# Optimization experiments

Hardware: AMD Instinct MI355X
Metric: run time of the kernel (lower is better)

## Reference

```python
import jax, jax.numpy as jnp
import numpy as np

N_NODES = 100000
N_EDGES = 1600000
D_IN, D_HID, D_OUT = 64, 64, 32


def _glorot(key, shape):
    fan_in, fan_out = shape[0], shape[1]
    lim = np.sqrt(6.0 / (fan_in + fan_out)).astype(np.float32)
    return jax.random.uniform(key, shape, jnp.float32, -lim, lim)


def setup_inputs() -> dict:
    key = jax.random.key(0)
    ks = jax.random.split(key, 12)
    x = jax.random.normal(ks[0], (N_NODES, D_IN), jnp.float32)
    edge_index = jax.random.randint(ks[1], (2, N_EDGES), 0, N_NODES, jnp.int64)
    return {
        "x": x,
        "edge_index": edge_index,
        # SAGEConv 1 (in->hid): lin_l (aggregated neighbors, with bias), lin_r (root, no bias)
        "Wl1": _glorot(ks[2], (D_IN, D_HID)),
        "Wr1": _glorot(ks[3], (D_IN, D_HID)),
        "b1": jnp.zeros((D_HID,), jnp.float32),
        # SAGEConv 2 (hid->out)
        "Wl2": _glorot(ks[4], (D_HID, D_OUT)),
        "Wr2": _glorot(ks[5], (D_HID, D_OUT)),
        "b2": jnp.zeros((D_OUT,), jnp.float32),
        # trust head: Linear(32,16) -> ReLU -> Linear(16,1) -> Sigmoid (dropout inert in eval)
        "Wt1": _glorot(ks[6], (D_OUT, 16)),
        "bt1": jnp.zeros((16,), jnp.float32),
        "Wt2": _glorot(ks[7], (16, 1)),
        "bt2": jnp.zeros((1,), jnp.float32),
    }


def _sage_conv(x, src, dst, Wl, Wr, b):
    # mean-aggregate neighbor messages: msg flows src -> dst
    msg = x[src]                                              # [E, d] gather
    agg_sum = jax.ops.segment_sum(msg, dst, num_segments=N_NODES)
    deg = jax.ops.segment_sum(jnp.ones((src.shape[0],), x.dtype), dst,
                              num_segments=N_NODES)
    agg = agg_sum / jnp.maximum(deg, 1.0)[:, None]            # zero-degree -> 0
    return agg @ Wl + x @ Wr + b


def reference(x, edge_index, Wl1, Wr1, b1, Wl2, Wr2, b2, Wt1, bt1, Wt2, bt2):
    src, dst = edge_index[0], edge_index[1]
    h = _sage_conv(x, src, dst, Wl1, Wr1, b1)
    h = jax.nn.relu(h)                    # dropout p=0.3 inert in eval
    h = _sage_conv(h, src, dst, Wl2, Wr2, b2)
    t = jax.nn.relu(h @ Wt1 + bt1)        # dropout p=0.2 inert in eval
    trust = jax.nn.sigmoid(t @ Wt2 + bt2)
    return h, trust
```

## Files before the change

### kernel.cpp

```cpp
#include <hip/hip_runtime.h>
#include <math.h>


#define NBUCK   1563
#define BCAP    1536
#define BKCHUNK 4096

__device__ inline unsigned short f2bf(float x) {
    unsigned u = __float_as_uint(x);
    unsigned r = u + 0x7fffu + ((u >> 16) & 1u);
    return (unsigned short)(r >> 16);
}
__device__ inline unsigned pack2(float a, float b) {
    return (unsigned)f2bf(a) | ((unsigned)f2bf(b) << 16);
}
__device__ inline float bflo(unsigned u) { return __uint_as_float(u << 16); }
__device__ inline float bfhi(unsigned u) { return __uint_as_float(u & 0xffff0000u); }

__global__ __launch_bounds__(256) void k_m1(
    const float* __restrict__ x,
    const float* __restrict__ Wl1, const float* __restrict__ Wr1,
    const float* __restrict__ b1,
    unsigned* __restrict__ u16b, float* __restrict__ v,
    const int* __restrict__ src, const int* __restrict__ dst,
    int* __restrict__ gcnt, unsigned* __restrict__ pairs,
    int N, int E, int GB, int BKB)
{
    __shared__ __align__(16) char smem[33792];
    int tid = threadIdx.x;
    int g = blockIdx.x / 5, r5 = blockIdx.x % 5;

    if (r5 == 4) {
        if (g >= BKB) return;
        int* hist = (int*)smem;
        int e0 = g * BKCHUNK;
        int e1 = min(e0 + BKCHUNK, E);

        for (int i = tid; i < NBUCK; i += 256) hist[i] = 0;
        __syncthreads();
        for (int e = e0 + tid; e < e1; e += 256)
            atomicAdd(&hist[((unsigned)dst[e]) >> 6], 1);
        __syncthreads();
        for (int i = tid; i < NBUCK; i += 256)
            if (hist[i] > 0)
                hist[i] = i * BCAP + atomicAdd(&gcnt[i], hist[i]);
        __syncthreads();
        for (int e = e0 + tid; e < e1; e += 256) {
            int t = dst[e];
            int b = ((unsigned)t) >> 6;
            int pos = atomicAdd(&hist[b], 1);
            if (pos < (b + 1) * BCAP)
                pairs[pos] = (unsigned)src[e] | ((unsigned)(t & 63) << 17);
        }
        return;
    }

    int tile = 4 * g + r5;
    if (tile >= GB) return;
    float* sXT = (float*)smem;
    float* sW  = (float*)(smem + 17408);
    int nblk = tile * 64;

    for (int i = tid * 4; i < 64 * 64; i += 1024) {
        int r = i >> 6, c = i & 63;
        int node = nblk + r;
        float4 xv = (node < N) ? *(const float4*)&x[(size_t)node * 64 + c]
                               : make_float4(0.f, 0.f, 0.f, 0.f);
        sXT[(c + 0) * 68 + r] = xv.x;
        sXT[(c + 1) * 68 + r] = xv.y;
        sXT[(c + 2) * 68 + r] = xv.z;
        sXT[(c + 3) * 68 + r] = xv.w;
    }

    int mg = tid >> 4, ng = tid & 15;
    int m0 = mg * 4, n0 = ng * 4;

    #pragma unroll
    for (int pass = 0; pass < 2; ++pass) {
        const float* W = pass ? Wr1 : Wl1;
        if (pass) __syncthreads();
        for (int i = tid * 4; i < 64 * 64; i += 1024)
            *(float4*)&sW[i] = *(const float4*)&W[i];
        __syncthreads();

        float acc[4][4];
        #pragma unroll
        for (int mi = 0; mi < 4; ++mi)
            #pragma unroll
            for (int ni = 0; ni < 4; ++ni) acc[mi][ni] = 0.0f;

        #pragma unroll 8
        for (int k = 0; k < 64; ++k) {
            float4 a = *(float4*)&sXT[k * 68 + m0];
            float4 w = *(float4*)&sW[k * 64 + n0];
            float av[4] = {a.x, a.y, a.z, a.w};
            float wv[4] = {w.x, w.y, w.z, w.w};
            #pragma unroll
            for (int mi = 0; mi < 4; ++mi)
                #pragma unroll
                for (int ni = 0; ni < 4; ++ni)
                    acc[mi][ni] = fmaf(av[mi], wv[ni], acc[mi][ni]);
        }

        if (pass == 0) {
            #pragma unroll
            for (int mi = 0; mi < 4; ++mi) {
                int node = nblk + m0 + mi;
                if (node >= N) continue;
                uint2 pk;
                pk.x = pack2(acc[mi][0], acc[mi][1]);
                pk.y = pack2(acc[mi][2], acc[mi][3]);
                *(uint2*)&u16b[(size_t)node * 32 + (n0 >> 1)] = pk;
            }
        } else {
            float4 b0 = *(const float4*)&b1[n0];
            #pragma unroll
            for (int mi = 0; mi < 4; ++mi) {
                int node = nblk + m0 + mi;
                if (node >= N) continue;
                *(float4*)&v[(size_t)node * 64 + n0] =
                    make_float4(acc[mi][0]+b0.x, acc[mi][1]+b0.y,
                                acc[mi][2]+b0.z, acc[mi][3]+b0.w);
            }
        }
    }
}

__global__ __launch_bounds__(512) void k_m2(
    const unsigned* __restrict__ pairs, const int* __restrict__ gcnt,
    const unsigned* __restrict__ u16b, const float* __restrict__ v,
    const float* __restrict__ Wl2, const float* __restrict__ Wr2,
    const float* __restrict__ b2,
    unsigned* __restrict__ P16b, float* __restrict__ Qout,
    int2* __restrict__ nodeOff, int* __restrict__ adjG, int N)
{
    __shared__ float sH[64 * 66];
    __shared__ float sW[64 * 64];
    __shared__ int   sAdj[BCAP];
    __shared__ int   sOff[65];
    __shared__ int   sCur[64];
    int tid = threadIdx.x;
    int b = blockIdx.x;
    int nodeBase = b * 64;
    int base = b * BCAP;
    int count = min(gcnt[b], BCAP);
    const unsigned* pp = pairs + (size_t)b * BCAP;

    for (int i = tid * 4; i < 64 * 64; i += 2048) {
        int k = i >> 6, n = i & 63;
        const float* Wsrc = (n < 32) ? (Wl2 + k * 32 + n) : (Wr2 + k * 32 + (n - 32));
        *(float4*)&sW[k * 64 + n] = *(const float4*)Wsrc;
    }
    if (tid < 64) sCur[tid] = 0;
    __syncthreads();

    for (int j = tid; j < count; j += 512)
        atomicAdd(&sCur[(pp[j] >> 17) & 63], 1);
    __syncthreads();
    if (tid < 64) {
        int c = sCur[tid];
        int incl = c;
        #pragma unroll
        for (int off = 1; off < 64; off <<= 1) {
            int t = __shfl_up(incl, off);
            if (tid >= off) incl += t;
        }
        sOff[tid] = incl - c;
        if (tid == 63) sOff[64] = incl;
    }
    __syncthreads();
    if (tid < 64) {
        sCur[tid] = sOff[tid];
        int node = nodeBase + tid;
        if (node < N)
            nodeOff[node] = make_int2(base + sOff[tid], sOff[tid + 1] - sOff[tid]);
    }
    __syncthreads();
    for (int j = tid; j < count; j += 512) {
        unsigned e = pp[j];
        int pos = atomicAdd(&sCur[(e >> 17) & 63], 1);
        sAdj[pos] = (int)(e & 0x1FFFFu);
    }
    __syncthreads();
    for (int j = tid; j < count; j += 512) adjG[base + j] = sAdj[j];

    int hw = tid >> 5, lane = tid & 31;
    for (int r = 0; r < 4; ++r) {
        int nl = hw * 4 + r;
        int node = nodeBase + nl;
        float h0 = 0.0f, h1v = 0.0f;
        if (node < N) {
            int beg = sOff[nl], end = sOff[nl + 1];
            float lo[8] = {0,0,0,0,0,0,0,0}, hi[8] = {0,0,0,0,0,0,0,0};
            int i = beg;
            for (; i + 8 <= end; i += 8) {
                int s[8];
                #pragma unroll
                for (int j = 0; j < 8; ++j) s[j] = sAdj[i + j];
                #pragma unroll
                for (int j = 0; j < 8; ++j) {
                    unsigned w = u16b[(size_t)s[j] * 32 + lane];
                    lo[j] += bflo(w); hi[j] += bfhi(w);
                }
            }
            for (; i < end; ++i) {
                unsigned w = u16b[(size_t)sAdj[i] * 32 + lane];
                lo[0] += bflo(w); hi[0] += bfhi(w);
            }
            float mlo = ((lo[0]+lo[1])+(lo[2]+lo[3])) + ((lo[4]+lo[5])+(lo[6]+lo[7]));
            float mhi = ((hi[0]+hi[1])+(hi[2]+hi[3])) + ((hi[4]+hi[5])+(hi[6]+hi[7]));
            int deg = end - beg;
            float invd = (deg > 0) ? 1.0f / (float)deg : 1.0f;
            float2 vv = ((const float2*)v)[(size_t)node * 32 + lane];
            h0  = fmaxf(mlo * invd + vv.x, 0.0f);
            h1v = fmaxf(mhi * invd + vv.y, 0.0f);
        }
        *(float2*)&sH[nl * 66 + 2 * lane] = make_float2(h0, h1v);
    }
    __syncthreads();

    int ng = tid & 15;
    int mg = tid >> 4;
    int m0 = mg * 2, n0 = ng * 4;

    float acc[2][4];
    #pragma unroll
    for (int mi = 0; mi < 2; ++mi)
        #pragma unroll
        for (int ni = 0; ni < 4; ++ni) acc[mi][ni] = 0.0f;

    #pragma unroll 8
    for (int k = 0; k < 64; ++k) {
        float a0 = sH[(m0 + 0) * 66 + k];
        float a1 = sH[(m0 + 1) * 66 + k];
        float4 w = *(float4*)&sW[k * 64 + n0];
        float wv[4] = {w.x, w.y, w.z, w.w};
        #pragma unroll
        for (int ni = 0; ni < 4; ++ni) {
            acc[0][ni] = fmaf(a0, wv[ni], acc[0][ni]);
            acc[1][ni] = fmaf(a1, wv[ni], acc[1][ni]);
        }
    }

    if (n0 < 32) {
        #pragma unroll
        for (int mi = 0; mi < 2; ++mi) {
            int node = nodeBase + m0 + mi;
            if (node >= N) continue;
            uint2 pk;
            pk.x = pack2(acc[mi][0], acc[mi][1]);
            pk.y = pack2(acc[mi][2], acc[mi][3]);
            *(uint2*)&P16b[(size_t)node * 16 + (n0 >> 1)] = pk;
        }
    } else {
        float4 b0 = *(const float4*)&b2[n0 - 32];
        #pragma unroll
        for (int mi = 0; mi < 2; ++mi) {
            int node = nodeBase + m0 + mi;
            if (node >= N) continue;
            *(float4*)&Qout[(size_t)node * 32 + (n0 - 32)] =
                make_float4(acc[mi][0]+b0.x, acc[mi][1]+b0.y,
                            acc[mi][2]+b0.z, acc[mi][3]+b0.w);
        }
    }
}

__global__ __launch_bounds__(256) void k_a2(
    const int2* __restrict__ nodeOff, const int* __restrict__ adj,
    const unsigned* __restrict__ P16b, const float* __restrict__ Q,
    const float* __restrict__ Wt1, const float* __restrict__ bt1,
    const float* __restrict__ Wt2, const float* __restrict__ bt2,
    float* __restrict__ out_h, float* __restrict__ out_trust, int N)
{
    __shared__ float sWt1[32 * 16];
    __shared__ float sWt2[16];
    for (int i = threadIdx.x; i < 512; i += 256) sWt1[i] = Wt1[i];
    if (threadIdx.x < 16) sWt2[threadIdx.x] = Wt2[threadIdx.x];
    __syncthreads();

    int n = blockIdx.x * 16 + (threadIdx.x >> 4);
    int lane = threadIdx.x & 15;
    if (n >= N) return;

    int2 od = nodeOff[n];
    int beg = od.x, end = od.x + od.y;
    float lo[8] = {0,0,0,0,0,0,0,0}, hi[8] = {0,0,0,0,0,0,0,0};
    int i = beg;
    for (; i + 8 <= end; i += 8) {
        int s[8];
        #pragma unroll
        for (int j = 0; j < 8; ++j) s[j] = adj[i + j];
        #pragma unroll
        for (int j = 0; j < 8; ++j) {
            unsigned w = P16b[(size_t)s[j] * 16 + lane];
            lo[j] += bflo(w); hi[j] += bfhi(w);
        }
    }
    for (; i < end; ++i) {
        unsigned w = P16b[(size_t)adj[i] * 16 + lane];
        lo[0] += bflo(w); hi[0] += bfhi(w);
    }
    float invd = (od.y > 0) ? 1.0f / (float)od.y : 1.0f;
    float mlo = (((lo[0]+lo[1])+(lo[2]+lo[3])) + ((lo[4]+lo[5])+(lo[6]+lo[7]))) * invd;
    float mhi = (((hi[0]+hi[1])+(hi[2]+hi[3])) + ((hi[4]+hi[5])+(hi[6]+hi[7]))) * invd;

    float2 qv = ((const float2*)Q)[(size_t)n * 16 + lane];
    float hx = mlo + qv.x;
    float hy = mhi + qv.y;

    ((float2*)out_h)[(size_t)n * 16 + lane] = make_float2(hx, hy);

    float t = bt1[lane];
    #pragma unroll
    for (int k = 0; k < 16; ++k) {
        float hlo = __shfl(hx, k, 16);
        float hhi = __shfl(hy, k, 16);
        t += hlo * sWt1[(2 * k) * 16 + lane] + hhi * sWt1[(2 * k + 1) * 16 + lane];
    }
    t = fmaxf(t, 0.0f);
    float z = t * sWt2[lane];
    z += __shfl_xor(z, 1);
    z += __shfl_xor(z, 2);
    z += __shfl_xor(z, 4);
    z += __shfl_xor(z, 8);
    if (lane == 0) out_trust[n] = 1.0f / (1.0f + expf(-(z + bt2[0])));
}


extern "C" void kernel_launch(void* const* d_in, const int* in_sizes, int n_in,
                              void* d_out, int out_size, void* d_ws, size_t ws_size,
                              hipStream_t stream)
{
    const float* x   = (const float*)d_in[0];
    const int*   ei  = (const int*)d_in[1];
    const float* Wl1 = (const float*)d_in[2];
    const float* Wr1 = (const float*)d_in[3];
    const float* b1  = (const float*)d_in[4];
    const float* Wl2 = (const float*)d_in[5];
    const float* Wr2 = (const float*)d_in[6];
    const float* b2  = (const float*)d_in[7];
    const float* Wt1 = (const float*)d_in[8];
    const float* bt1 = (const float*)d_in[9];
    const float* Wt2 = (const float*)d_in[10];
    const float* bt2 = (const float*)d_in[11];

    const int N = in_sizes[0] / 64;
    const int E = in_sizes[1] / 2;
    const int* src = ei;
    const int* dst = ei + E;

    unsigned* pairs  = (unsigned*)d_ws;
    unsigned* u16b   = pairs + (size_t)NBUCK * BCAP;
    float*    v      = (float*)(u16b + (size_t)N * 32);
    unsigned* P16b   = (unsigned*)(v + (size_t)N * 64);
    float*    Q      = (float*)(P16b + (size_t)N * 16);
    int2*     nodeOff= (int2*)(Q + (size_t)N * 32);
    int*      adj    = (int*)(nodeOff + N);
    int*      gcnt   = adj + (size_t)NBUCK * BCAP;

    hipMemsetAsync(gcnt, 0, 2048 * sizeof(int), stream);

    const int GB  = (N + 63) / 64;
    const int BKB = (E + BKCHUNK - 1) / BKCHUNK;
    int grp = (GB + 3) / 4 > BKB ? (GB + 3) / 4 : BKB;
    k_m1<<<5 * grp, 256, 0, stream>>>(x, Wl1, Wr1, b1, u16b, v,
                                      src, dst, gcnt, pairs, N, E, GB, BKB);
    k_m2<<<NBUCK, 512, 0, stream>>>(pairs, gcnt, u16b, v, Wl2, Wr2, b2,
                                    P16b, Q, nodeOff, adj, N);

    float* out_h     = (float*)d_out;
    float* out_trust = out_h + (size_t)N * 32;
    k_a2<<<(N + 15) / 16, 256, 0, stream>>>(nodeOff, adj, P16b, Q,
                                            Wt1, bt1, Wt2, bt2,
                                            out_h, out_trust, N);
}
```

Measured before the change: 234.2 us.

## Use split-bf16 MFMA for first-layer node projections in k_m1

Replaces the scalar FMA 64x64 tile GEMM in k_m1 with bf16 MFMA 16x16x32 instructions. Inputs and weights are split into hi and lo bf16 parts, and three MFMAs per k-fragment approximate fp32 accuracy. Both weight matrices are staged transposed in shared memory once, instead of being reloaded per pass. Output stores become 2- or 4-byte scattered writes per lane rather than vectorised ones, which may cost memory efficiency, and precision changes slightly.

New measurement: 233.0 us. No clear change (-0.5%).

```diff
diff --git a/kernel.cpp b/kernel.cpp
--- a/kernel.cpp
+++ b/kernel.cpp
@@ -5,6 +5,11 @@
 #define NBUCK   1563
 #define BCAP    1536
 #define BKCHUNK 4096
+
+typedef __attribute__((ext_vector_type(8))) __bf16 bf16x8;
+typedef __attribute__((ext_vector_type(4))) float  f32x4;
+
+union BU { bf16x8 v; unsigned short u[8]; };
 
 __device__ inline unsigned short f2bf(float x) {
     unsigned u = __float_as_uint(x);
@@ -16,6 +21,7 @@
 }
 __device__ inline float bflo(unsigned u) { return __uint_as_float(u << 16); }
 __device__ inline float bfhi(unsigned u) { return __uint_as_float(u & 0xffff0000u); }
+__device__ inline float bf2f(unsigned short h) { return __uint_as_float((unsigned)h << 16); }
 
 __global__ __launch_bounds__(256) void k_m1(
     const float* __restrict__ x,
@@ -26,7 +32,7 @@
     int* __restrict__ gcnt, unsigned* __restrict__ pairs,
     int N, int E, int GB, int BKB)
 {
-    __shared__ __align__(16) char smem[33792];
+    __shared__ __align__(16) char smem[36864];
     int tid = threadIdx.x;
     int g = blockIdx.x / 5, r5 = blockIdx.x % 5;
 
@@ -57,70 +63,90 @@
 
     int tile = 4 * g + r5;
     if (tile >= GB) return;
-    float* sXT = (float*)smem;
-    float* sW  = (float*)(smem + 17408);
+    unsigned short* sW = (unsigned short*)smem;
+    const int PL = 64 * 72;
     int nblk = tile * 64;
 
     for (int i = tid * 4; i < 64 * 64; i += 1024) {
-        int r = i >> 6, c = i & 63;
-        int node = nblk + r;
-        float4 xv = (node < N) ? *(const float4*)&x[(size_t)node * 64 + c]
-                               : make_float4(0.f, 0.f, 0.f, 0.f);
-        sXT[(c + 0) * 68 + r] = xv.x;
-        sXT[(c + 1) * 68 + r] = xv.y;
-        sXT[(c + 2) * 68 + r] = xv.z;
-        sXT[(c + 3) * 68 + r] = xv.w;
-    }
-
-    int mg = tid >> 4, ng = tid & 15;
-    int m0 = mg * 4, n0 = ng * 4;
+        int k = i >> 6, n = i & 63;
+        float4 a  = *(const float4*)&Wl1[i];
+        float4 bq = *(const float4*)&Wr1[i];
+        float av[4] = {a.x, a.y, a.z, a.w};
+        float bv[4] = {bq.x, bq.y, bq.z, bq.w};
+        #pragma unroll
+        for (int j = 0; j < 4; ++j) {
+            unsigned short h0 = f2bf(av[j]);
+            unsigned short l0 = f2bf(av[j] - bf2f(h0));
+            unsigned short h1 = f2bf(bv[j]);
+            unsigned short l1 = f2bf(bv[j] - bf2f(h1));
+            int o = (n + j) * 72 + k;
+            sW[0 * PL + o] = h0; sW[1 * PL + o] = l0;
+            sW[2 * PL + o] = h1; sW[3 * PL + o] = l1;
+        }
+    }
+    __syncthreads();
+
+    int l  = tid & 63, wv = tid >> 6;
+    int la = l & 15,   g4 = l >> 4;
+    int arow = nblk + wv * 16 + la;
+    bool rowOK = (arow < N);
+
+    BU ahi[2], alo[2];
+    #pragma unroll
+    for (int kf = 0; kf < 2; ++kf) {
+        float xv[8];
+        if (rowOK) {
+            const float* xp = &x[(size_t)arow * 64 + kf * 32 + g4 * 8];
+            float4 p0 = *(const float4*)xp;
+            float4 p1 = *(const float4*)(xp + 4);
+            xv[0] = p0.x; xv[1] = p0.y; xv[2] = p0.z; xv[3] = p0.w;
+            xv[4] = p1.x; xv[5] = p1.y; xv[6] = p1.z; xv[7] = p1.w;
+        } else {
+            #pragma unroll
+            for (int e = 0; e < 8; ++e) xv[e] = 0.0f;
+        }
+        #pragma unroll
+        for (int e = 0; e < 8; ++e) {
+            unsigned short h = f2bf(xv[e]);
+            ahi[kf].u[e] = h;
+            alo[kf].u[e] = f2bf(xv[e] - bf2f(h));
+        }
+    }
+
+    unsigned short* u16 = (unsigned short*)u16b;
 
     #pragma unroll
     for (int pass = 0; pass < 2; ++pass) {
-        const float* W = pass ? Wr1 : Wl1;
-        if (pass) __syncthreads();
-        for (int i = tid * 4; i < 64 * 64; i += 1024)
-            *(float4*)&sW[i] = *(const float4*)&W[i];
-        __syncthreads();
-
-        float acc[4][4];
-        #pragma unroll
-        for (int mi = 0; mi < 4; ++mi)
+        const unsigned short* Whi = sW + (pass ? 2 : 0) * PL;
+        const unsigned short* Wlo = sW + (pass ? 3 : 1) * PL;
+        #pragma unroll
+        for (int nf = 0; nf < 4; ++nf) {
+            int n0 = nf * 16;
+            f32x4 acc = {0.f, 0.f, 0.f, 0.f};
             #pragma unroll
-            for (int ni = 0; ni < 4; ++ni) acc[mi][ni] = 0.0f;
-
-        #pragma unroll 8
-        for (int k = 0; k < 64; ++k) {
-            float4 a = *(float4*)&sXT[k * 68 + m0];
-            float4 w = *(float4*)&sW[k * 64 + n0];
-            float av[4] = {a.x, a.y, a.z, a.w};
-            float wv[4] = {w.x, w.y, w.z, w.w};
-            #pragma unroll
-            for (int mi = 0; mi < 4; ++mi)
+            for (int kf = 0; kf < 2; ++kf) {
+                int off = (n0 + la) * 72 + kf * 32 + g4 * 8;
+                bf16x8 bhi = *(const bf16x8*)&Whi[off];
+                bf16x8 blo = *(const bf16x8*)&Wlo[off];
+                acc = __builtin_amdgcn_mfma_f32_16x16x32_bf16(ahi[kf].v, bhi, acc, 0, 0, 0);
+                acc = __builtin_amdgcn_mfma_f32_16x16x32_bf16(alo[kf].v, bhi, acc, 0, 0, 0);
+                acc = __builtin_amdgcn_mfma_f32_16x16x32_bf16(ahi[kf].v, blo, acc, 0, 0, 0);
+            }
+            if (pass == 0) {
                 #pragma unroll
-                for (int ni = 0; ni < 4; ++ni)
-                    acc[mi][ni] = fmaf(av[mi], wv[ni], acc[mi][ni]);
-        }
-
-        if (pass == 0) {
-            #pragma unroll
-            for (int mi = 0; mi < 4; ++mi) {
-                int node = nblk + m0 + mi;
-                if (node >= N) continue;
-                uint2 pk;
-                pk.x = pack2(acc[mi][0], acc[mi][1]);
-                pk.y = pack2(acc[mi][2], acc[mi][3]);
-                *(uint2*)&u16b[(size_t)node * 32 + (n0 >> 1)] = pk;
-            }
-        } else {
-            float4 b0 = *(const float4*)&b1[n0];
-            #pragma unroll
-            for (int mi = 0; mi < 4; ++mi) {
-                int node = nblk + m0 + mi;
-                if (node >= N) continue;
-                *(float4*)&v[(size_t)node * 64 + n0] =
-                    make_float4(acc[mi][0]+b0.x, acc[mi][1]+b0.y,
-                                acc[mi][2]+b0.z, acc[mi][3]+b0.w);
+                for (int r = 0; r < 4; ++r) {
+                    int nd = nblk + wv * 16 + g4 * 4 + r;
+                    if (nd < N)
+                        u16[(size_t)nd * 64 + n0 + la] = f2bf(acc[r]);
+                }
+            } else {
+                float bb = b1[n0 + la];
+                #pragma unroll
+                for (int r = 0; r < 4; ++r) {
+                    int nd = nblk + wv * 16 + g4 * 4 + r;
+                    if (nd < N)
+                        v[(size_t)nd * 64 + n0 + la] = acc[r] + bb;
+                }
             }
         }
     }
```
